# Performance work log

Measured on AMD Instinct MI355X. Metric: run time of the kernel, lower is better.

Reference implementation:

```python
import jax, jax.numpy as jnp
import numpy as np
import math

N_GENES_TOTAL = 5000   # full gene table (fragments.n_genes)
N_CELLS_TOTAL = 10000  # full cell count (libsize buffer)
NBINS = 128            # spline components per gene
N_LATENT = 64
B = 256                # n_cells in minibatch
G = 2000               # genes_oi
NCUTS = 500_000


def setup_inputs() -> dict:
    key = jax.random.key(0)
    ks = jax.random.split(key, 12)
    latent = jax.random.normal(ks[0], (B, N_LATENT), jnp.float32)
    genes_oi = jax.random.randint(ks[1], (G,), 0, N_GENES_TOTAL)
    cells_oi = jax.random.randint(ks[2], (B,), 0, N_CELLS_TOTAL)
    cut_coordinates = jax.random.uniform(ks[3], (NCUTS,), jnp.float32)
    cut_local_cellxgene_ix = jax.random.randint(ks[4], (NCUTS,), 0, B * G)
    cut_local_gene_ix = jax.random.randint(ks[5], (NCUTS,), 0, G)
    local_cellxgene_ix = jax.random.randint(ks[6], (NCUTS,), 0, B * G)
    s = 1.0 / math.sqrt(N_LATENT)
    logit_weight = jax.random.uniform(ks[7], (N_GENES_TOTAL, N_LATENT, NBINS), jnp.float32, -s, s)
    rho_weight = jax.random.uniform(ks[8], (N_GENES_TOTAL, N_LATENT), jnp.float32, -s / 100.0, s / 100.0)
    rho_bias = jax.random.uniform(ks[9], (N_GENES_TOTAL,), jnp.float32, 1e-4, 1e-2)
    libsize = jax.random.randint(ks[10], (N_CELLS_TOTAL,), 1000, 20000)
    spline_heights = 0.01 * jax.random.normal(ks[11], (N_GENES_TOTAL, NBINS), jnp.float32)
    return {
        "latent": latent, "genes_oi": genes_oi, "cells_oi": cells_oi,
        "cut_coordinates": cut_coordinates,
        "cut_local_cellxgene_ix": cut_local_cellxgene_ix,
        "cut_local_gene_ix": cut_local_gene_ix,
        "local_cellxgene_ix": local_cellxgene_ix,
        "logit_weight": logit_weight, "rho_weight": rho_weight,
        "rho_bias": rho_bias, "libsize": libsize,
        "spline_heights": spline_heights,
        "n_cells": B, "n_genes": G,
    }


def reference(latent, genes_oi, cells_oi, cut_coordinates,
              cut_local_cellxgene_ix, cut_local_gene_ix, local_cellxgene_ix,
              logit_weight, rho_weight, rho_bias, libsize, spline_heights,
              n_cells, n_genes):
    # Decoder with n_layers=0: nn is identity
    lw = logit_weight[genes_oi]                     # [G, L, C]
    rw = rho_weight[genes_oi]                       # [G, L]
    mixture_delta = jnp.einsum('bl,glc->bgc', latent, lw)   # [B, G, C]
    rho_delta = latent @ rw.T                       # [B, G]

    # gather per-cut mixture deltas
    delta_flat = mixture_delta.reshape(n_cells * n_genes, -1)
    delta_cut = delta_flat[cut_local_cellxgene_ix]  # [Ncuts, C]

    # spline/mixture log-likelihood: per-gene histogram density with delta
    gene_heights = spline_heights[genes_oi]         # [G, C]
    h = gene_heights[cut_local_gene_ix] + delta_cut  # [Ncuts, C]
    logp_bins = jax.nn.log_softmax(h, axis=-1)
    nbins = h.shape[-1]
    bin_ix = jnp.clip((cut_coordinates * nbins).astype(jnp.int32), 0, nbins - 1)
    likelihood_mixture = (
        jnp.take_along_axis(logp_bins, bin_ix[:, None], axis=-1)[:, 0]
        + jnp.log(jnp.float32(nbins))
    )

    # Poisson fragment-count likelihood
    rate = (rho_bias[genes_oi][None, :] * jnp.exp(rho_delta)
            * libsize[cells_oi].astype(jnp.float32)[:, None])   # [B, G]
    counts = jnp.bincount(local_cellxgene_ix, length=n_cells * n_genes)
    counts = counts.reshape(n_cells, n_genes).astype(jnp.float32)
    ll_counts = counts * jnp.log(rate) - rate - jax.scipy.special.gammaln(counts + 1.0)

    likelihood = likelihood_mixture.sum() + ll_counts.sum()
    return -likelihood
```

## Files before the change

### kernel.cpp

```cpp
#include <hip/hip_runtime.h>

#define LDIM 64
#define CDIM 128
#define MAXPER 512
#define LOG128 4.8520302639196171f

typedef __attribute__((ext_vector_type(8))) short bfrag;
typedef __attribute__((ext_vector_type(4))) float f32x4;

static __device__ __forceinline__ unsigned short f2bf(float f) {
    unsigned int x = __float_as_uint(f);
    unsigned int r = (x + 0x7fffu + ((x >> 16) & 1u)) >> 16;
    return (unsigned short)r;
}
static __device__ __forceinline__ float bf2f(unsigned int u) {
    return __uint_as_float(u << 16);
}

__global__ __launch_bounds__(256) void zero_kernel(uint4* __restrict__ p, size_t n16,
                                                   float* __restrict__ out, int out_size) {
    size_t i = (size_t)blockIdx.x * blockDim.x + threadIdx.x;
    size_t stride = (size_t)gridDim.x * blockDim.x;
    for (; i < n16; i += stride) p[i] = make_uint4(0u, 0u, 0u, 0u);
    if (blockIdx.x == 0 && threadIdx.x < (unsigned)out_size) out[threadIdx.x] = 0.f;
}

__global__ __launch_bounds__(256) void prep1_kernel(
    const float* __restrict__ heights, unsigned short* __restrict__ hbf, int nheights,
    const float* __restrict__ latent, unsigned short* __restrict__ latbf, int nlat,
    const int* __restrict__ cut_pair, const int* __restrict__ cut_gene,
    const float* __restrict__ coord, const int* __restrict__ genes_oi,
    const int* __restrict__ local_cxg, unsigned int* __restrict__ bucket_cnt,
    unsigned int* __restrict__ bucket, unsigned int* __restrict__ countsT,
    int ncuts, int B, int G, int N) {
    int stride = gridDim.x * blockDim.x;
    for (int i = blockIdx.x * blockDim.x + threadIdx.x; i < N; i += stride) {
        if (i < nheights) hbf[i] = f2bf(heights[i]);
        if (i < nlat) latbf[i] = f2bf(latent[i]);
        if (i < ncuts) {
            unsigned int p = (unsigned int)cut_pair[i];
            unsigned int g = p % (unsigned int)G;
            unsigned int cell = p / (unsigned int)G;
            unsigned int gg = (unsigned int)genes_oi[cut_gene[i]];
            int bin = (int)(coord[i] * 128.0f);
            bin = min(max(bin, 0), 127);
            unsigned int slot = atomicAdd(&bucket_cnt[g], 1u);
            if (slot < MAXPER)
                bucket[g * MAXPER + slot] = (cell << 24) | (gg << 7) | (unsigned int)bin;
            unsigned int q = (unsigned int)local_cxg[i];
            atomicAdd(&countsT[(q % (unsigned int)G) * (unsigned int)B +
                               (q / (unsigned int)G)], 1u);
        }
    }
}

__global__ __launch_bounds__(512, 2) void fused_kernel(
    const float* __restrict__ latent, const unsigned short* __restrict__ latbf,
    const int* __restrict__ genes_oi, const float* __restrict__ logit_weight,
    const unsigned short* __restrict__ hbf, const unsigned int* __restrict__ bucket,
    const unsigned int* __restrict__ bucket_cnt,
    const unsigned int* __restrict__ countsT, const int* __restrict__ cells_oi,
    const float* __restrict__ rho_weight, const float* __restrict__ rho_bias,
    const int* __restrict__ libsize, int B, int G, float* __restrict__ out) {
    __shared__ unsigned short dlds[256 * CDIM];
    __shared__ unsigned short blds[CDIM * LDIM];
    int t = threadIdx.x;
    int g = blockIdx.x;
    int gene = genes_oi[g];

    {
        int n = t & 127;
        int k0 = (t >> 7) * 16;
        const float* src = logit_weight + (size_t)gene * LDIM * CDIM;
        float v[16];
        #pragma unroll
        for (int j = 0; j < 16; ++j) v[j] = src[(size_t)(k0 + j) * CDIM + n];
        #pragma unroll
        for (int h = 0; h < 2; ++h) {
            union { unsigned short u[8]; uint4 q; } pk;
            #pragma unroll
            for (int j = 0; j < 8; ++j) pk.u[j] = f2bf(v[h * 8 + j]);
            int kk = k0 + h * 8;
            *(uint4*)(blds + n * LDIM + (kk ^ ((n & 7) * 8))) = pk.q;
        }
    }
    __syncthreads();

    int wv = t >> 6, ln = t & 63;
    int l15 = ln & 15, l4 = ln >> 4;
    f32x4 acc[2][8];
    #pragma unroll
    for (int m = 0; m < 2; ++m)
        #pragma unroll
        for (int n = 0; n < 8; ++n) acc[m][n] = (f32x4){0.f, 0.f, 0.f, 0.f};

    #pragma unroll
    for (int ks = 0; ks < 2; ++ks) {
        int kk = ks * 32 + l4 * 8;
        bfrag a0 = *(const bfrag*)(latbf + (wv * 32 + l15) * LDIM + kk);
        bfrag a1 = *(const bfrag*)(latbf + (wv * 32 + 16 + l15) * LDIM + kk);
        #pragma unroll
        for (int n = 0; n < 8; ++n) {
            int col = n * 16 + l15;
            bfrag b = *(const bfrag*)(blds + col * LDIM + (kk ^ ((col & 7) * 8)));
            acc[0][n] = __builtin_amdgcn_mfma_f32_16x16x32_bf16(a0, b, acc[0][n], 0, 0, 0);
            acc[1][n] = __builtin_amdgcn_mfma_f32_16x16x32_bf16(a1, b, acc[1][n], 0, 0, 0);
        }
    }
    #pragma unroll
    for (int m = 0; m < 2; ++m)
        #pragma unroll
        for (int n = 0; n < 8; ++n)
            #pragma unroll
            for (int r = 0; r < 4; ++r) {
                int row = wv * 32 + m * 16 + l4 * 4 + r;
                int col = n * 16 + l15;
                dlds[row * CDIM + (col ^ ((row & 7) * 8))] = f2bf(acc[m][n][r]);
            }
    __syncthreads();

    float accs = 0.f;
    {
        unsigned int cnt = bucket_cnt[g];
        if (cnt > MAXPER) cnt = MAXPER;
        const unsigned int* bk = bucket + (size_t)g * MAXPER;
        int grp = t >> 4, sub = t & 15;
        for (unsigned int i = (unsigned int)grp; i < cnt; i += 32u) {
            unsigned int r = bk[i];
            int row = (int)(r >> 24);
            unsigned int gg = (r >> 7) & 0x1FFFu;
            uint4 dv = *(const uint4*)(dlds + row * CDIM + ((sub * 8) ^ ((row & 7) * 8)));
            uint4 hv = *(const uint4*)(hbf + ((size_t)gg << 7) + sub * 8);
            float h0 = bf2f(hv.x & 0xffffu) + bf2f(dv.x & 0xffffu);
            float h1 = bf2f(hv.x >> 16)     + bf2f(dv.x >> 16);
            float h2 = bf2f(hv.y & 0xffffu) + bf2f(dv.y & 0xffffu);
            float h3 = bf2f(hv.y >> 16)     + bf2f(dv.y >> 16);
            float h4 = bf2f(hv.z & 0xffffu) + bf2f(dv.z & 0xffffu);
            float h5 = bf2f(hv.z >> 16)     + bf2f(dv.z >> 16);
            float h6 = bf2f(hv.w & 0xffffu) + bf2f(dv.w & 0xffffu);
            float h7 = bf2f(hv.w >> 16)     + bf2f(dv.w >> 16);
            float m = fmaxf(fmaxf(fmaxf(h0, h1), fmaxf(h2, h3)),
                            fmaxf(fmaxf(h4, h5), fmaxf(h6, h7)));
            #pragma unroll
            for (int o = 1; o < 16; o <<= 1) m = fmaxf(m, __shfl_xor(m, o));
            float s = __expf(h0 - m) + __expf(h1 - m) + __expf(h2 - m) + __expf(h3 - m)
                    + __expf(h4 - m) + __expf(h5 - m) + __expf(h6 - m) + __expf(h7 - m);
            #pragma unroll
            for (int o = 1; o < 16; o <<= 1) s += __shfl_xor(s, o);
            int bin = (int)(r & 127u);
            int e = bin & 7;
            float sel = h0;
            sel = (e == 1) ? h1 : sel;
            sel = (e == 2) ? h2 : sel;
            sel = (e == 3) ? h3 : sel;
            sel = (e == 4) ? h4 : sel;
            sel = (e == 5) ? h5 : sel;
            sel = (e == 6) ? h6 : sel;
            sel = (e == 7) ? h7 : sel;
            float hsel = __shfl(sel, (ln & 48) | (bin >> 3));
            if (sub == 0) accs += hsel - (m + __logf(s)) + LOG128;
        }
    }

    if (t < B) {
        const float4* la = (const float4*)(latent + (size_t)t * LDIM);
        const float4* rw = (const float4*)(rho_weight + (size_t)gene * LDIM);
        float d = 0.f;
        #pragma unroll
        for (int k = 0; k < LDIM / 4; ++k) {
            float4 a = la[k], w = rw[k];
            d += a.x * w.x + a.y * w.y + a.z * w.z + a.w * w.w;
        }
        float rb = rho_bias[gene];
        float lib = (float)libsize[cells_oi[t]];
        float lrate = __logf(rb) + d + __logf(lib);
        float rate = __expf(lrate);
        unsigned int c = countsT[(size_t)g * B + t];
        float lgam = 0.f;
        for (unsigned int k = 2; k <= c; ++k) lgam += __logf((float)k);
        accs += (float)c * lrate - rate - lgam;
    }

    #pragma unroll
    for (int o = 32; o; o >>= 1) accs += __shfl_xor(accs, o);
    __syncthreads();
    float* red = (float*)blds;
    if (ln == 0) red[wv] = accs;
    __syncthreads();
    if (t == 0) {
        float s = red[0] + red[1] + red[2] + red[3] + red[4] + red[5] + red[6] + red[7];
        atomicAdd(out, -s);
    }
}

extern "C" void kernel_launch(void* const* d_in, const int* in_sizes, int n_in,
                              void* d_out, int out_size, void* d_ws, size_t ws_size,
                              hipStream_t stream) {
    const float* latent         = (const float*)d_in[0];
    const int*   genes_oi       = (const int*)d_in[1];
    const int*   cells_oi       = (const int*)d_in[2];
    const float* cut_coord      = (const float*)d_in[3];
    const int*   cut_pair       = (const int*)d_in[4];
    const int*   cut_gene       = (const int*)d_in[5];
    const int*   local_cxg      = (const int*)d_in[6];
    const float* logit_weight   = (const float*)d_in[7];
    const float* rho_weight     = (const float*)d_in[8];
    const float* rho_bias       = (const float*)d_in[9];
    const int*   libsize        = (const int*)d_in[10];
    const float* spline_heights = (const float*)d_in[11];
    int G = in_sizes[1];
    int B = in_sizes[2];
    int ncuts = in_sizes[4];
    int nheights = in_sizes[11];
    int nlat = B * LDIM;

    char* ws = (char*)d_ws;
    size_t off = 0;
    unsigned int* countsT = (unsigned int*)(ws + off);
    off += ((size_t)B * G * 4 + 255) & ~(size_t)255;
    unsigned int* bucket_cnt = (unsigned int*)(ws + off);
    off += ((size_t)G * 4 + 255) & ~(size_t)255;
    size_t zero_bytes = off;
    unsigned int* bucket = (unsigned int*)(ws + off);
    off += ((size_t)G * MAXPER * 4 + 255) & ~(size_t)255;
    unsigned short* hbf = (unsigned short*)(ws + off);
    off += ((size_t)nheights * 2 + 255) & ~(size_t)255;
    unsigned short* latbf = (unsigned short*)(ws + off);
    off += ((size_t)nlat * 2 + 255) & ~(size_t)255;

    float* out = (float*)d_out;
    zero_kernel<<<1024, 256, 0, stream>>>((uint4*)ws, zero_bytes / 16, out, out_size);

    int N = ncuts > nheights ? ncuts : nheights;
    prep1_kernel<<<2048, 256, 0, stream>>>(
        spline_heights, hbf, nheights, latent, latbf, nlat,
        cut_pair, cut_gene, cut_coord, genes_oi, local_cxg,
        bucket_cnt, bucket, countsT, ncuts, B, G, N);
    fused_kernel<<<G, 512, 0, stream>>>(
        latent, latbf, genes_oi, logit_weight, hbf, bucket,
        bucket_cnt, countsT, cells_oi,
        rho_weight, rho_bias, libsize, B, G, out);
}
```

Measured before the change: 164.3 us.

## Replace dense counts matrix with per-gene cell buckets histogrammed in LDS

```diff
diff --git a/kernel.cpp b/kernel.cpp
--- a/kernel.cpp
+++ b/kernel.cpp
@@ -31,16 +31,17 @@
     const int* __restrict__ cut_pair, const int* __restrict__ cut_gene,
     const float* __restrict__ coord, const int* __restrict__ genes_oi,
     const int* __restrict__ local_cxg, unsigned int* __restrict__ bucket_cnt,
-    unsigned int* __restrict__ bucket, unsigned int* __restrict__ countsT,
-    int ncuts, int B, int G, int N) {
+    unsigned int* __restrict__ bucket, unsigned int* __restrict__ cnt2,
+    unsigned char* __restrict__ bucket2,
+    int ncuts, int B, int G, int N, unsigned int magicG) {
     int stride = gridDim.x * blockDim.x;
     for (int i = blockIdx.x * blockDim.x + threadIdx.x; i < N; i += stride) {
         if (i < nheights) hbf[i] = f2bf(heights[i]);
         if (i < nlat) latbf[i] = f2bf(latent[i]);
         if (i < ncuts) {
             unsigned int p = (unsigned int)cut_pair[i];
-            unsigned int g = p % (unsigned int)G;
-            unsigned int cell = p / (unsigned int)G;
+            unsigned int cell = __umulhi(p, magicG);
+            unsigned int g = p - cell * (unsigned int)G;
             unsigned int gg = (unsigned int)genes_oi[cut_gene[i]];
             int bin = (int)(coord[i] * 128.0f);
             bin = min(max(bin, 0), 127);
@@ -48,8 +49,11 @@
             if (slot < MAXPER)
                 bucket[g * MAXPER + slot] = (cell << 24) | (gg << 7) | (unsigned int)bin;
             unsigned int q = (unsigned int)local_cxg[i];
-            atomicAdd(&countsT[(q % (unsigned int)G) * (unsigned int)B +
-                               (q / (unsigned int)G)], 1u);
+            unsigned int cell2 = __umulhi(q, magicG);
+            unsigned int g2 = q - cell2 * (unsigned int)G;
+            unsigned int slot2 = atomicAdd(&cnt2[g2], 1u);
+            if (slot2 < MAXPER)
+                bucket2[g2 * MAXPER + slot2] = (unsigned char)cell2;
         }
     }
 }
@@ -59,7 +63,8 @@
     const int* __restrict__ genes_oi, const float* __restrict__ logit_weight,
     const unsigned short* __restrict__ hbf, const unsigned int* __restrict__ bucket,
     const unsigned int* __restrict__ bucket_cnt,
-    const unsigned int* __restrict__ countsT, const int* __restrict__ cells_oi,
+    const unsigned int* __restrict__ cnt2, const unsigned char* __restrict__ bucket2,
+    const int* __restrict__ cells_oi,
     const float* __restrict__ rho_weight, const float* __restrict__ rho_bias,
     const int* __restrict__ libsize, int B, int G, float* __restrict__ out) {
     __shared__ unsigned short dlds[256 * CDIM];
@@ -118,6 +123,19 @@
                 dlds[row * CDIM + (col ^ ((row & 7) * 8))] = f2bf(acc[m][n][r]);
             }
     __syncthreads();
+
+    unsigned int* lcnt = (unsigned int*)blds;
+    float* red = (float*)(blds + 2048);
+    if (t < 256) lcnt[t] = 0u;
+    __syncthreads();
+
+    {
+        unsigned int c2 = cnt2[g];
+        if (c2 > MAXPER) c2 = MAXPER;
+        const unsigned char* b2 = bucket2 + (size_t)g * MAXPER;
+        for (unsigned int i = (unsigned int)t; i < c2; i += 512u)
+            atomicAdd(&lcnt[b2[i]], 1u);
+    }
 
     float accs = 0.f;
     {
@@ -161,6 +179,7 @@
             if (sub == 0) accs += hsel - (m + __logf(s)) + LOG128;
         }
     }
+    __syncthreads();
 
     if (t < B) {
         const float4* la = (const float4*)(latent + (size_t)t * LDIM);
@@ -175,7 +194,7 @@
         float lib = (float)libsize[cells_oi[t]];
         float lrate = __logf(rb) + d + __logf(lib);
         float rate = __expf(lrate);
-        unsigned int c = countsT[(size_t)g * B + t];
+        unsigned int c = lcnt[t];
         float lgam = 0.f;
         for (unsigned int k = 2; k <= c; ++k) lgam += __logf((float)k);
         accs += (float)c * lrate - rate - lgam;
@@ -184,7 +203,6 @@
     #pragma unroll
     for (int o = 32; o; o >>= 1) accs += __shfl_xor(accs, o);
     __syncthreads();
-    float* red = (float*)blds;
     if (ln == 0) red[wv] = accs;
     __syncthreads();
     if (t == 0) {
@@ -213,31 +231,34 @@
     int ncuts = in_sizes[4];
     int nheights = in_sizes[11];
     int nlat = B * LDIM;
+    unsigned int magicG = (unsigned int)((0x100000000ULL + (unsigned)G - 1) / (unsigned)G);
 
     char* ws = (char*)d_ws;
     size_t off = 0;
-    unsigned int* countsT = (unsigned int*)(ws + off);
-    off += ((size_t)B * G * 4 + 255) & ~(size_t)255;
     unsigned int* bucket_cnt = (unsigned int*)(ws + off);
+    off += ((size_t)G * 4 + 255) & ~(size_t)255;
+    unsigned int* cnt2 = (unsigned int*)(ws + off);
     off += ((size_t)G * 4 + 255) & ~(size_t)255;
     size_t zero_bytes = off;
     unsigned int* bucket = (unsigned int*)(ws + off);
     off += ((size_t)G * MAXPER * 4 + 255) & ~(size_t)255;
+    unsigned char* bucket2 = (unsigned char*)(ws + off);
+    off += ((size_t)G * MAXPER + 255) & ~(size_t)255;
     unsigned short* hbf = (unsigned short*)(ws + off);
     off += ((size_t)nheights * 2 + 255) & ~(size_t)255;
     unsigned short* latbf = (unsigned short*)(ws + off);
     off += ((size_t)nlat * 2 + 255) & ~(size_t)255;
 
     float* out = (float*)d_out;
-    zero_kernel<<<1024, 256, 0, stream>>>((uint4*)ws, zero_bytes / 16, out, out_size);
+    zero_kernel<<<16, 256, 0, stream>>>((uint4*)ws, zero_bytes / 16, out, out_size);
 
     int N = ncuts > nheights ? ncuts : nheights;
     prep1_kernel<<<2048, 256, 0, stream>>>(
         spline_heights, hbf, nheights, latent, latbf, nlat,
         cut_pair, cut_gene, cut_coord, genes_oi, local_cxg,
-        bucket_cnt, bucket, countsT, ncuts, B, G, N);
+        bucket_cnt, bucket, cnt2, bucket2, ncuts, B, G, N, magicG);
     fused_kernel<<<G, 512, 0, stream>>>(
         latent, latbf, genes_oi, logit_weight, hbf, bucket,
-        bucket_cnt, countsT, cells_oi,
+        bucket_cnt, cnt2, bucket2, cells_oi,
         rho_weight, rho_bias, libsize, B, G, out);
 }
```

After: 202.5 us. 1.23x slower.

## Replicate per-gene bucket counters across block groups and use magic-number division

Applied to the files above, without the earlier changes.

```diff
diff --git a/kernel.cpp b/kernel.cpp
--- a/kernel.cpp
+++ b/kernel.cpp
@@ -2,7 +2,9 @@
 
 #define LDIM 64
 #define CDIM 128
-#define MAXPER 512
+#define NREP 8
+#define SUBCAP 64
+#define MAXPER (NREP * SUBCAP)
 #define LOG128 4.8520302639196171f
 
 typedef __attribute__((ext_vector_type(8))) short bfrag;
@@ -30,26 +32,29 @@
     const float* __restrict__ latent, unsigned short* __restrict__ latbf, int nlat,
     const int* __restrict__ cut_pair, const int* __restrict__ cut_gene,
     const float* __restrict__ coord, const int* __restrict__ genes_oi,
-    const int* __restrict__ local_cxg, unsigned int* __restrict__ bucket_cnt,
+    const int* __restrict__ local_cxg, unsigned int* __restrict__ cnt_rep,
     unsigned int* __restrict__ bucket, unsigned int* __restrict__ countsT,
-    int ncuts, int B, int G, int N) {
+    int ncuts, int B, int G, int N, unsigned int magicG) {
     int stride = gridDim.x * blockDim.x;
+    int rep = blockIdx.x & (NREP - 1);
     for (int i = blockIdx.x * blockDim.x + threadIdx.x; i < N; i += stride) {
         if (i < nheights) hbf[i] = f2bf(heights[i]);
         if (i < nlat) latbf[i] = f2bf(latent[i]);
         if (i < ncuts) {
             unsigned int p = (unsigned int)cut_pair[i];
-            unsigned int g = p % (unsigned int)G;
-            unsigned int cell = p / (unsigned int)G;
+            unsigned int cell = __umulhi(p, magicG);
+            unsigned int g = p - cell * (unsigned int)G;
             unsigned int gg = (unsigned int)genes_oi[cut_gene[i]];
             int bin = (int)(coord[i] * 128.0f);
             bin = min(max(bin, 0), 127);
-            unsigned int slot = atomicAdd(&bucket_cnt[g], 1u);
-            if (slot < MAXPER)
-                bucket[g * MAXPER + slot] = (cell << 24) | (gg << 7) | (unsigned int)bin;
+            unsigned int slot = atomicAdd(&cnt_rep[rep * G + (int)g], 1u);
+            if (slot < SUBCAP)
+                bucket[g * MAXPER + rep * SUBCAP + slot] =
+                    (cell << 24) | (gg << 7) | (unsigned int)bin;
             unsigned int q = (unsigned int)local_cxg[i];
-            atomicAdd(&countsT[(q % (unsigned int)G) * (unsigned int)B +
-                               (q / (unsigned int)G)], 1u);
+            unsigned int cell2 = __umulhi(q, magicG);
+            unsigned int g2 = q - cell2 * (unsigned int)G;
+            atomicAdd(&countsT[(size_t)g2 * (unsigned int)B + cell2], 1u);
         }
     }
 }
@@ -58,8 +63,8 @@
     const float* __restrict__ latent, const unsigned short* __restrict__ latbf,
     const int* __restrict__ genes_oi, const float* __restrict__ logit_weight,
     const unsigned short* __restrict__ hbf, const unsigned int* __restrict__ bucket,
-    const unsigned int* __restrict__ bucket_cnt,
-    const unsigned int* __restrict__ countsT, const int* __restrict__ cells_oi,
+    const unsigned int* __restrict__ cnt_rep, const unsigned int* __restrict__ countsT,
+    const int* __restrict__ cells_oi,
     const float* __restrict__ rho_weight, const float* __restrict__ rho_bias,
     const int* __restrict__ libsize, int B, int G, float* __restrict__ out) {
     __shared__ unsigned short dlds[256 * CDIM];
@@ -121,44 +126,48 @@
 
     float accs = 0.f;
     {
-        unsigned int cnt = bucket_cnt[g];
-        if (cnt > MAXPER) cnt = MAXPER;
         const unsigned int* bk = bucket + (size_t)g * MAXPER;
         int grp = t >> 4, sub = t & 15;
-        for (unsigned int i = (unsigned int)grp; i < cnt; i += 32u) {
-            unsigned int r = bk[i];
-            int row = (int)(r >> 24);
-            unsigned int gg = (r >> 7) & 0x1FFFu;
-            uint4 dv = *(const uint4*)(dlds + row * CDIM + ((sub * 8) ^ ((row & 7) * 8)));
-            uint4 hv = *(const uint4*)(hbf + ((size_t)gg << 7) + sub * 8);
-            float h0 = bf2f(hv.x & 0xffffu) + bf2f(dv.x & 0xffffu);
-            float h1 = bf2f(hv.x >> 16)     + bf2f(dv.x >> 16);
-            float h2 = bf2f(hv.y & 0xffffu) + bf2f(dv.y & 0xffffu);
-            float h3 = bf2f(hv.y >> 16)     + bf2f(dv.y >> 16);
-            float h4 = bf2f(hv.z & 0xffffu) + bf2f(dv.z & 0xffffu);
-            float h5 = bf2f(hv.z >> 16)     + bf2f(dv.z >> 16);
-            float h6 = bf2f(hv.w & 0xffffu) + bf2f(dv.w & 0xffffu);
-            float h7 = bf2f(hv.w >> 16)     + bf2f(dv.w >> 16);
-            float m = fmaxf(fmaxf(fmaxf(h0, h1), fmaxf(h2, h3)),
-                            fmaxf(fmaxf(h4, h5), fmaxf(h6, h7)));
-            #pragma unroll
-            for (int o = 1; o < 16; o <<= 1) m = fmaxf(m, __shfl_xor(m, o));
-            float s = __expf(h0 - m) + __expf(h1 - m) + __expf(h2 - m) + __expf(h3 - m)
-                    + __expf(h4 - m) + __expf(h5 - m) + __expf(h6 - m) + __expf(h7 - m);
-            #pragma unroll
-            for (int o = 1; o < 16; o <<= 1) s += __shfl_xor(s, o);
-            int bin = (int)(r & 127u);
-            int e = bin & 7;
-            float sel = h0;
-            sel = (e == 1) ? h1 : sel;
-            sel = (e == 2) ? h2 : sel;
-            sel = (e == 3) ? h3 : sel;
-            sel = (e == 4) ? h4 : sel;
-            sel = (e == 5) ? h5 : sel;
-            sel = (e == 6) ? h6 : sel;
-            sel = (e == 7) ? h7 : sel;
-            float hsel = __shfl(sel, (ln & 48) | (bin >> 3));
-            if (sub == 0) accs += hsel - (m + __logf(s)) + LOG128;
+        #pragma unroll
+        for (int r = 0; r < NREP; ++r) {
+            unsigned int cr = cnt_rep[r * G + g];
+            if (cr > SUBCAP) cr = SUBCAP;
+            const unsigned int* bs = bk + r * SUBCAP;
+            for (unsigned int i = (unsigned int)grp; i < cr; i += 32u) {
+                unsigned int rc = bs[i];
+                int row = (int)(rc >> 24);
+                unsigned int gg = (rc >> 7) & 0x1FFFu;
+                uint4 dv = *(const uint4*)(dlds + row * CDIM + ((sub * 8) ^ ((row & 7) * 8)));
+                uint4 hv = *(const uint4*)(hbf + ((size_t)gg << 7) + sub * 8);
+                float h0 = bf2f(hv.x & 0xffffu) + bf2f(dv.x & 0xffffu);
+                float h1 = bf2f(hv.x >> 16)     + bf2f(dv.x >> 16);
+                float h2 = bf2f(hv.y & 0xffffu) + bf2f(dv.y & 0xffffu);
+                float h3 = bf2f(hv.y >> 16)     + bf2f(dv.y >> 16);
+                float h4 = bf2f(hv.z & 0xffffu) + bf2f(dv.z & 0xffffu);
+                float h5 = bf2f(hv.z >> 16)     + bf2f(dv.z >> 16);
+                float h6 = bf2f(hv.w & 0xffffu) + bf2f(dv.w & 0xffffu);
+                float h7 = bf2f(hv.w >> 16)     + bf2f(dv.w >> 16);
+                float m = fmaxf(fmaxf(fmaxf(h0, h1), fmaxf(h2, h3)),
+                                fmaxf(fmaxf(h4, h5), fmaxf(h6, h7)));
+                #pragma unroll
+                for (int o = 1; o < 16; o <<= 1) m = fmaxf(m, __shfl_xor(m, o));
+                float s = __expf(h0 - m) + __expf(h1 - m) + __expf(h2 - m) + __expf(h3 - m)
+                        + __expf(h4 - m) + __expf(h5 - m) + __expf(h6 - m) + __expf(h7 - m);
+                #pragma unroll
+                for (int o = 1; o < 16; o <<= 1) s += __shfl_xor(s, o);
+                int bin = (int)(rc & 127u);
+                int e = bin & 7;
+                float sel = h0;
+                sel = (e == 1) ? h1 : sel;
+                sel = (e == 2) ? h2 : sel;
+                sel = (e == 3) ? h3 : sel;
+                sel = (e == 4) ? h4 : sel;
+                sel = (e == 5) ? h5 : sel;
+                sel = (e == 6) ? h6 : sel;
+                sel = (e == 7) ? h7 : sel;
+                float hsel = __shfl(sel, (ln & 48) | (bin >> 3));
+                if (sub == 0) accs += hsel - (m + __logf(s)) + LOG128;
+            }
         }
     }
 
@@ -213,13 +222,14 @@
     int ncuts = in_sizes[4];
     int nheights = in_sizes[11];
     int nlat = B * LDIM;
+    unsigned int magicG = (unsigned int)((0x100000000ULL + (unsigned)G - 1) / (unsigned)G);
 
     char* ws = (char*)d_ws;
     size_t off = 0;
     unsigned int* countsT = (unsigned int*)(ws + off);
     off += ((size_t)B * G * 4 + 255) & ~(size_t)255;
-    unsigned int* bucket_cnt = (unsigned int*)(ws + off);
-    off += ((size_t)G * 4 + 255) & ~(size_t)255;
+    unsigned int* cnt_rep = (unsigned int*)(ws + off);
+    off += ((size_t)G * NREP * 4 + 255) & ~(size_t)255;
     size_t zero_bytes = off;
     unsigned int* bucket = (unsigned int*)(ws + off);
     off += ((size_t)G * MAXPER * 4 + 255) & ~(size_t)255;
@@ -235,9 +245,9 @@
     prep1_kernel<<<2048, 256, 0, stream>>>(
         spline_heights, hbf, nheights, latent, latbf, nlat,
         cut_pair, cut_gene, cut_coord, genes_oi, local_cxg,
-        bucket_cnt, bucket, countsT, ncuts, B, G, N);
+        cnt_rep, bucket, countsT, ncuts, B, G, N, magicG);
     fused_kernel<<<G, 512, 0, stream>>>(
         latent, latbf, genes_oi, logit_weight, hbf, bucket,
-        bucket_cnt, countsT, cells_oi,
+        cnt_rep, countsT, cells_oi,
         rho_weight, rho_bias, libsize, B, G, out);
 }
```

New measurement: 135.2 us. -17.7%, faster.
